# Optimization experiments

Measured on AMD Instinct MI355X. Metric: run time of the kernel, lower is better.

The kernel has to match this reference:

```python
import jax, jax.numpy as jnp
import numpy as np

B, A, T, NMODE, H = 4, 16, 32, 8, 256
NSCENE = 512
HEADS = 8
FF = 128
LN_EPS = 1e-6

def _layer_norm(x, g, b, eps=LN_EPS):
    mu = jnp.mean(x, axis=-1, keepdims=True)
    var = jnp.mean((x - mu) ** 2, axis=-1, keepdims=True)
    return (x - mu) * jax.lax.rsqrt(var + eps) * g + b


def setup_inputs() -> dict:
    key = jax.random.key(0)
    ks = jax.random.split(key, 16)
    s = 1.0 / np.sqrt(H)
    sf = 1.0 / np.sqrt(FF)
    return {
        "hidden_vecs": jax.random.normal(ks[0], (B, A, T, NMODE, H), jnp.float32),
        "scene_hidden_vec": jax.random.normal(ks[1], (B, NSCENE, H), jnp.float32),
        # nn.MultiheadAttention packed in_proj: rows [Wq; Wk; Wv]
        "in_proj_w": jax.random.normal(ks[2], (3 * H, H), jnp.float32) * s,
        "in_proj_b": jnp.zeros((3 * H,), jnp.float32),
        "out_proj_w": jax.random.normal(ks[3], (H, H), jnp.float32) * s,
        "out_proj_b": jnp.zeros((H,), jnp.float32),
        "attn_ln_g": jnp.ones((H,), jnp.float32),
        "attn_ln_b": jnp.zeros((H,), jnp.float32),
        "ff1_w": jax.random.normal(ks[4], (FF, H), jnp.float32) * s,
        "ff1_b": jnp.zeros((FF,), jnp.float32),
        "ff2_w": jax.random.normal(ks[5], (H, FF), jnp.float32) * sf,
        "ff2_b": jnp.zeros((H,), jnp.float32),
        "ff_ln_g": jnp.ones((H,), jnp.float32),
        "ff_ln_b": jnp.zeros((H,), jnp.float32),
    }


def reference(hidden_vecs, scene_hidden_vec, in_proj_w, in_proj_b, out_proj_w,
              out_proj_b, attn_ln_g, attn_ln_b, ff1_w, ff1_b, ff2_w, ff2_b,
              ff_ln_g, ff_ln_b):
    b, a, t, n, h = hidden_vecs.shape
    N = scene_hidden_vec.shape[1]
    d = h // HEADS
    m = a * t * n  # queries per batch element

    Wq, Wk, Wv = in_proj_w[:h], in_proj_w[h:2 * h], in_proj_w[2 * h:]
    bq, bk, bv = in_proj_b[:h], in_proj_b[h:2 * h], in_proj_b[2 * h:]

    # Project queries; K/V computed ONCE per batch (shared across a,t,n) --
    # avoids materializing the (b,a,t,n,N,h) expanded tensor.
    q = (hidden_vecs.reshape(b, m, h) @ Wq.T + bq).reshape(b, m, HEADS, d)
    k = (scene_hidden_vec @ Wk.T + bk).reshape(b, N, HEADS, d)
    v = (scene_hidden_vec @ Wv.T + bv).reshape(b, N, HEADS, d)

    scale = 1.0 / np.sqrt(d)
    scores = jnp.einsum('bmed,bned->bemn', q * scale, k)  # (b, heads, m, N)
    attn = jax.nn.softmax(scores, axis=-1)
    ctx = jnp.einsum('bemn,bned->bmed', attn, v).reshape(b, m, h)
    attn_out = (ctx @ out_proj_w.T + out_proj_b).reshape(b, a, t, n, h)

    # averaged attention weights over heads (average_attn_weights=True)
    attn_score = jnp.mean(attn, axis=1).reshape(b, a, t, n, 1, N)

    x = _layer_norm(attn_out + hidden_vecs, attn_ln_g, attn_ln_b)
    ff = jax.nn.relu(x @ ff1_w.T + ff1_b) @ ff2_w.T + ff2_b
    out = _layer_norm(ff + x, ff_ln_g, ff_ln_b)
    return out, attn_score
```

## Files before the change

kernel.cpp:

```cpp
#include <hip/hip_runtime.h>
#include <hip/hip_bf16.h>

#define H 256
#define NSC 512
#define MQ 4096
#define BATCH 4

typedef __attribute__((ext_vector_type(8))) short bf16x8;
typedef __attribute__((ext_vector_type(4))) float f32x4;

__device__ __forceinline__ ushort f2bf(float x) {
    union { float f; unsigned u; } c; c.f = x;
    unsigned r = c.u + 0x7FFF + ((c.u >> 16) & 1);
    return (ushort)(r >> 16);
}
__device__ __forceinline__ unsigned pk2(float hi, float lo) {
    union { float f; unsigned u; } a, b; a.f = hi; b.f = lo;
    return __builtin_amdgcn_perm(a.u, b.u, 0x07060302u);
}
__device__ __forceinline__ uint4 cvt8f(const float* p) {
    float4 a = *(const float4*)p;
    float4 b = *(const float4*)(p + 4);
    uint4 r;
    r.x = pk2(a.y, a.x); r.y = pk2(a.w, a.z);
    r.z = pk2(b.y, b.x); r.w = pk2(b.w, b.z);
    return r;
}
#define EXP2(x) __builtin_amdgcn_exp2f(x)

template<int MODE>
__device__ __forceinline__ void gemm_body(
    ushort* As, ushort* Bs, int bx, int by,
    const float* __restrict__ Ain, const float* __restrict__ W,
    const float* __restrict__ bias,
    void* __restrict__ out, ushort* __restrict__ out2,
    int K, int N, float alpha)
{
    const int t = threadIdx.x;
    const int w = t >> 6, lane = t & 63, g = lane >> 4, l15 = lane & 15;
    const int rowBase = by * 64;
    const int colBase = bx * 256;
    const int wr = (w >> 2) * 32;
    const int wc = (w & 3) * 64;
    f32x4 acc[2][4];
    #pragma unroll
    for (int mt = 0; mt < 2; mt++)
        #pragma unroll
        for (int nt = 0; nt < 4; nt++) acc[mt][nt] = (f32x4){0.f,0.f,0.f,0.f};

    const int sr = t >> 3, skc = t & 7, sp = skc ^ (sr & 7);
    const size_t arow = (size_t)(rowBase + sr) * K + skc * 8;

    uint4 av = cvt8f(Ain + arow);
    uint4 bv[4];
    #pragma unroll
    for (int i = 0; i < 4; i++) {
        const int u = t + 512*i, br = u >> 3, bkc = u & 7;
        int brow = colBase + br; if (brow > N - 1) brow = N - 1;
        bv[i] = cvt8f(W + (size_t)brow * K + bkc*8);
    }

    for (int k0 = 0; k0 < K; k0 += 64) {
        __syncthreads();
        *(uint4*)&As[sr*64 + sp*8] = av;
        #pragma unroll
        for (int i = 0; i < 4; i++) {
            const int u = t + 512*i, br = u >> 3, bkc = u & 7, bp = bkc ^ (br & 7);
            *(uint4*)&Bs[br*64 + bp*8] = bv[i];
        }
        __syncthreads();
        if (k0 + 64 < K) {
            av = cvt8f(Ain + arow + k0 + 64);
            #pragma unroll
            for (int i = 0; i < 4; i++) {
                const int u = t + 512*i, br = u >> 3, bkc = u & 7;
                int brow = colBase + br; if (brow > N - 1) brow = N - 1;
                bv[i] = cvt8f(W + (size_t)brow * K + k0 + 64 + bkc*8);
            }
        }
        #pragma unroll
        for (int kk = 0; kk < 2; kk++) {
            const int swz = ((kk*4 + g) ^ (l15 & 7)) * 8;
            bf16x8 af[2], bfr[4];
            #pragma unroll
            for (int mt = 0; mt < 2; mt++)
                af[mt] = *(const bf16x8*)&As[(wr + mt*16 + l15)*64 + swz];
            #pragma unroll
            for (int nt = 0; nt < 4; nt++)
                bfr[nt] = *(const bf16x8*)&Bs[(wc + nt*16 + l15)*64 + swz];
            #pragma unroll
            for (int mt = 0; mt < 2; mt++)
                #pragma unroll
                for (int nt = 0; nt < 4; nt++)
                    acc[mt][nt] = __builtin_amdgcn_mfma_f32_16x16x32_bf16(
                        af[mt], bfr[nt], acc[mt][nt], 0, 0, 0);
        }
    }

    if (MODE == 0) {
        #pragma unroll
        for (int nt = 0; nt < 4; nt++) {
            const int col = colBase + wc + nt*16 + l15;
            if (col < N) {
                const float bb = bias[col];
                #pragma unroll
                for (int mt = 0; mt < 2; mt++)
                    #pragma unroll
                    for (int r = 0; r < 4; r++) {
                        const int row = rowBase + wr + mt*16 + g*4 + r;
                        float o = (acc[mt][nt][r] + bb) * alpha;
                        ((ushort*)out)[(size_t)row * N + col] = f2bf(o);
                    }
            }
        }
    } else {
        #pragma unroll
        for (int nt = 0; nt < 4; nt++) {
            const int col = colBase + wc + nt*16 + l15;
            const float bb = bias[col];
            #pragma unroll
            for (int mt = 0; mt < 2; mt++) {
                const int row0 = rowBase + wr + mt*16 + g*4;
                if (col < 256) {
                    #pragma unroll
                    for (int r = 0; r < 4; r++)
                        ((ushort*)out)[(size_t)(row0 + r) * 256 + col] = f2bf(acc[mt][nt][r] + bb);
                } else {
                    ushort4 pkv = { f2bf(acc[mt][nt][0] + bb), f2bf(acc[mt][nt][1] + bb),
                                    f2bf(acc[mt][nt][2] + bb), f2bf(acc[mt][nt][3] + bb) };
                    *(ushort4*)&out2[(size_t)((row0 >> 9)*256 + col - 256) * 512 + (row0 & 511)] = pkv;
                }
            }
        }
    }
}

__global__ __launch_bounds__(512, 4) void qkv_kernel(
    const float* __restrict__ hidden, const float* __restrict__ scene,
    const float* __restrict__ in_w, const float* __restrict__ in_b,
    ushort* __restrict__ qb, ushort* __restrict__ kb, ushort* __restrict__ vtb,
    float alpha_q)
{
    __shared__ ushort As[64 * 64];
    __shared__ ushort Bs[256 * 64];
    if (blockIdx.x < 256) {
        gemm_body<0>(As, Bs, 0, blockIdx.x, hidden, in_w, in_b,
                     qb, nullptr, 256, 256, alpha_q);
    } else {
        const int bid = blockIdx.x - 256;
        gemm_body<1>(As, Bs, bid >> 5, bid & 31, scene, in_w + 65536, in_b + 256,
                     kb, vtb, 256, 512, 1.f);
    }
}

__global__ __launch_bounds__(1024, 4) void mega_kernel(
    const ushort* __restrict__ q, const ushort* __restrict__ k,
    const ushort* __restrict__ vt,
    const float* __restrict__ Wo, const float* __restrict__ bo,
    const float* __restrict__ hid,
    const float* __restrict__ ag, const float* __restrict__ ab,
    const float* __restrict__ W1, const float* __restrict__ b1,
    const float* __restrict__ W2, const float* __restrict__ b2,
    const float* __restrict__ fg, const float* __restrict__ fbv,
    float* __restrict__ out, float* __restrict__ attn_score)
{
    __shared__ uint4 SHraw[8096];
    ushort* SH = (ushort*)SHraw;
    ushort* Ks = SH;
    ushort* Vs = SH + 8448;
    ushort* Pb = SH + 18688;
    ushort* Cb = SH + 39168;
    float*  Lg = (float*)(SH + 63744);
    ushort* Bs = SH;
    ushort* Xb = SH + 18688;
    float*  Ls = (float*)(SH + 35072);
    float*  Lq = (float*)(SH + 35584);
    ushort* Fb = SH + 55552;

    const int t = threadIdx.x;
    const int w = t >> 6, lane = t & 63, g = lane >> 4, l15 = lane & 15;
    const int b = blockIdx.x >> 6;
    const int m0 = (blockIdx.x & 63) * 64;
    const size_t rowG = (size_t)b * MQ + m0;
    const size_t kg = (size_t)b * NSC * H;
    const size_t vg = (size_t)b * H * NSC;

    const int hh0 = w & 7, hf = w >> 3;
    bf16x8 qf[2];
    #pragma unroll
    for (int qt = 0; qt < 2; qt++)
        qf[qt] = *(const bf16x8*)&q[(rowG + hf*32 + qt*16 + l15) * H + hh0*32 + g*8];

    f32x4 cacc[2][2];
    float lacc[2][4];
    #pragma unroll
    for (int qt = 0; qt < 2; qt++) {
        #pragma unroll
        for (int dt = 0; dt < 2; dt++) cacc[qt][dt] = (f32x4){0.f,0.f,0.f,0.f};
        #pragma unroll
        for (int r = 0; r < 4; r++) lacc[qt][r] = 0.f;
    }

    const int skey = t >> 5, spart = t & 31;
    const int sd = t >> 2, sp2 = t & 3;
    bf16x8 kr = *(const bf16x8*)&k[kg + (size_t)skey*H + spart*8];
    bf16x8 vr = *(const bf16x8*)&vt[vg + (size_t)sd*NSC + sp2*8];

    for (int c = 0; c < 16; c++) {
        const int kbase = c * 32;
        __syncthreads();
        *(bf16x8*)&Ks[skey*264 + spart*8] = kr;
        *(bf16x8*)&Vs[sd*40 + sp2*8] = vr;
        __syncthreads();
        if (c < 15) {
            kr = *(const bf16x8*)&k[kg + (size_t)(kbase + 32 + skey)*H + spart*8];
            vr = *(const bf16x8*)&vt[vg + (size_t)sd*NSC + kbase + 32 + sp2*8];
        }
        #pragma unroll
        for (int qt = 0; qt < 2; qt++) {
            #pragma unroll
            for (int kt = 0; kt < 2; kt++) {
                bf16x8 kf = *(const bf16x8*)&Ks[(kt*16 + l15)*264 + hh0*32 + g*8];
                f32x4 s = __builtin_amdgcn_mfma_f32_16x16x32_bf16(
                    qf[qt], kf, (f32x4){0.f,0.f,0.f,0.f}, 0, 0, 0);
                #pragma unroll
                for (int r = 0; r < 4; r++) {
                    float p = EXP2(s[r]);
                    lacc[qt][r] += p;
                    Pb[(w*32 + qt*16 + g*4 + r)*40 + kt*16 + l15] = f2bf(p);
                }
            }
        }
        #pragma unroll
        for (int qt = 0; qt < 2; qt++) {
            bf16x8 pf = *(const bf16x8*)&Pb[(w*32 + qt*16 + l15)*40 + g*8];
            #pragma unroll
            for (int dt = 0; dt < 2; dt++) {
                bf16x8 vf = *(const bf16x8*)&Vs[(hh0*32 + dt*16 + l15)*40 + g*8];
                cacc[qt][dt] = __builtin_amdgcn_mfma_f32_16x16x32_bf16(
                    pf, vf, cacc[qt][dt], 0, 0, 0);
            }
        }
    }

    #pragma unroll
    for (int qt = 0; qt < 2; qt++) {
        float invl[4];
        #pragma unroll
        for (int r = 0; r < 4; r++) {
            float v = lacc[qt][r];
            v += __shfl_xor(v, 1); v += __shfl_xor(v, 2);
            v += __shfl_xor(v, 4); v += __shfl_xor(v, 8);
            invl[r] = 1.f / v;
            if (l15 == 0) Lg[hh0*64 + hf*32 + qt*16 + g*4 + r] = -__log2f(v) - 3.0f;
        }
        #pragma unroll
        for (int dt = 0; dt < 2; dt++)
            #pragma unroll
            for (int r = 0; r < 4; r++) {
                const int qr = hf*32 + qt*16 + g*4 + r;
                const int col = hh0*32 + dt*16 + l15;
                Cb[qr*256 + (((col >> 3) ^ (qr & 7)) << 3) + (col & 7)]
                    = f2bf(cacc[qt][dt][r] * invl[r]);
            }
    }

    __syncthreads();

    {
        f32x4 sacc[4][2];
        #pragma unroll
        for (int qt = 0; qt < 4; qt++)
            #pragma unroll
            for (int kt = 0; kt < 2; kt++) sacc[qt][kt] = (f32x4){0.f,0.f,0.f,0.f};

        #pragma unroll 2
        for (int h = 0; h < 8; h++) {
            float lgq[4]; bf16x8 qv[4];
            #pragma unroll
            for (int qt = 0; qt < 4; qt++) {
                lgq[qt] = Lg[h*64 + qt*16 + l15];
                qv[qt] = *(const bf16x8*)&q[(rowG + qt*16 + l15) * H + h*32 + g*8];
            }
            #pragma unroll
            for (int kt = 0; kt < 2; kt++) {
                bf16x8 kf2 = *(const bf16x8*)&k[kg + (size_t)(w*32 + kt*16 + l15)*H + h*32 + g*8];
                #pragma unroll
                for (int qt = 0; qt < 4; qt++) {
                    f32x4 s = __builtin_amdgcn_mfma_f32_16x16x32_bf16(
                        kf2, qv[qt], (f32x4){0.f,0.f,0.f,0.f}, 0, 0, 0);
                    #pragma unroll
                    for (int r = 0; r < 4; r++) sacc[qt][kt][r] += EXP2(s[r] + lgq[qt]);
                }
            }
        }
        #pragma unroll
        for (int qt = 0; qt < 4; qt++)
            #pragma unroll
            for (int kt = 0; kt < 2; kt++)
                *(f32x4*)&attn_score[(rowG + qt*16 + l15)*NSC + w*32 + kt*16 + g*4]
                    = sacc[qt][kt];
    }

    const int wr = (w >> 2) * 16;
    const int wc = (w & 3) * 64;
    float xres[4][4];
    {
        f32x4 acc[4];
        #pragma unroll
        for (int nt = 0; nt < 4; nt++) acc[nt] = (f32x4){0.f,0.f,0.f,0.f};

        uint4 bv[2];
        #pragma unroll
        for (int i = 0; i < 2; i++) {
            const int u = t + 1024*i, br = u >> 3, bkc = u & 7;
            bv[i] = cvt8f(Wo + (size_t)br * 256 + bkc*8);
        }
        for (int k0 = 0; k0 < 256; k0 += 64) {
            __syncthreads();
            #pragma unroll
            for (int i = 0; i < 2; i++) {
                const int u = t + 1024*i, br = u >> 3, bkc = u & 7, bp = bkc ^ (br & 7);
                *(uint4*)&Bs[br*64 + bp*8] = bv[i];
            }
            __syncthreads();
            if (k0 < 192) {
                #pragma unroll
                for (int i = 0; i < 2; i++) {
                    const int u = t + 1024*i, br = u >> 3, bkc = u & 7;
                    bv[i] = cvt8f(Wo + (size_t)br * 256 + k0 + 64 + bkc*8);
                }
            }
            #pragma unroll
            for (int kk = 0; kk < 2; kk++) {
                const int rowC = wr + l15;
                const int gi = (k0 >> 3) + kk*4 + g;
                bf16x8 af = *(const bf16x8*)&Cb[rowC*256 + ((gi ^ (rowC & 7)) << 3)];
                const int swz = ((kk*4 + g) ^ (l15 & 7)) * 8;
                #pragma unroll
                for (int nt = 0; nt < 4; nt++) {
                    bf16x8 bfr = *(const bf16x8*)&Bs[(wc + nt*16 + l15)*64 + swz];
                    acc[nt] = __builtin_amdgcn_mfma_f32_16x16x32_bf16(
                        af, bfr, acc[nt], 0, 0, 0);
                }
            }
        }
        float bb[4], gmv[4], btv[4];
        #pragma unroll
        for (int nt = 0; nt < 4; nt++) {
            const int col = wc + nt*16 + l15;
            bb[nt] = bo[col]; gmv[nt] = ag[col]; btv[nt] = ab[col];
        }
        #pragma unroll
        for (int r = 0; r < 4; r++) {
            const float* rp = hid + (rowG + wr + g*4 + r) * 256;
            #pragma unroll
            for (int nt = 0; nt < 4; nt++)
                acc[nt][r] += bb[nt] + rp[wc + nt*16 + l15];
        }
        float ps[4], pq[4];
        #pragma unroll
        for (int r = 0; r < 4; r++) {
            float s = (acc[0][r] + acc[1][r]) + (acc[2][r] + acc[3][r]);
            float qq = (acc[0][r]*acc[0][r] + acc[1][r]*acc[1][r])
                     + (acc[2][r]*acc[2][r] + acc[3][r]*acc[3][r]);
            #pragma unroll
            for (int m = 1; m < 16; m <<= 1) {
                s += __shfl_xor(s, m);
                qq += __shfl_xor(qq, m);
            }
            ps[r] = s; pq[r] = qq;
        }
        if (l15 == 0) {
            #pragma unroll
            for (int r = 0; r < 4; r++) {
                const int ri = wr + g*4 + r;
                Ls[ri*4 + (w & 3)] = ps[r];
                Lq[ri*4 + (w & 3)] = pq[r];
            }
        }
        __syncthreads();
        #pragma unroll
        for (int r = 0; r < 4; r++) {
            const int ri = wr + g*4 + r;
            f32x4 sv = *(const f32x4*)&Ls[ri*4];
            f32x4 qv2 = *(const f32x4*)&Lq[ri*4];
            const float mu = (sv[0]+sv[1]+sv[2]+sv[3]) * (1.f/256.f);
            const float ex2 = (qv2[0]+qv2[1]+qv2[2]+qv2[3]) * (1.f/256.f);
            const float rs = rsqrtf(ex2 - mu*mu + 1e-6f);
            #pragma unroll
            for (int nt = 0; nt < 4; nt++) {
                const int col = wc + nt*16 + l15;
                const float o = (acc[nt][r] - mu) * rs * gmv[nt] + btv[nt];
                xres[nt][r] = o;
                Xb[ri*256 + (((col >> 3) ^ (ri & 7)) << 3) + (col & 7)] = f2bf(o);
            }
        }
    }

    {
        const int wrB = (w >> 2) * 16;
        const int wcB = (w & 3) * 32;
        f32x4 facc[2];
        #pragma unroll
        for (int nt = 0; nt < 2; nt++) facc[nt] = (f32x4){0.f,0.f,0.f,0.f};

        uint4 bv2 = cvt8f(W1 + (size_t)(t >> 3) * 256 + (t & 7)*8);
        for (int k0 = 0; k0 < 256; k0 += 64) {
            __syncthreads();
            {
                const int br = t >> 3, bkc = t & 7, bp = bkc ^ (br & 7);
                *(uint4*)&Bs[br*64 + bp*8] = bv2;
            }
            __syncthreads();
            if (k0 < 192)
                bv2 = cvt8f(W1 + (size_t)(t >> 3) * 256 + k0 + 64 + (t & 7)*8);
            #pragma unroll
            for (int kk = 0; kk < 2; kk++) {
                const int rowX = wrB + l15;
                const int gi = (k0 >> 3) + kk*4 + g;
                bf16x8 af = *(const bf16x8*)&Xb[rowX*256 + ((gi ^ (rowX & 7)) << 3)];
                const int swz = ((kk*4 + g) ^ (l15 & 7)) * 8;
                #pragma unroll
                for (int nt = 0; nt < 2; nt++) {
                    bf16x8 bfr = *(const bf16x8*)&Bs[(wcB + nt*16 + l15)*64 + swz];
                    facc[nt] = __builtin_amdgcn_mfma_f32_16x16x32_bf16(
                        af, bfr, facc[nt], 0, 0, 0);
                }
            }
        }
        #pragma unroll
        for (int nt = 0; nt < 2; nt++) {
            const int colF = wcB + nt*16 + l15;
            const float fbb = b1[colF];
            #pragma unroll
            for (int r = 0; r < 4; r++) {
                const int rowF = wrB + g*4 + r;
                const float o = fmaxf(facc[nt][r] + fbb, 0.f);
                Fb[rowF*128 + (((colF >> 3) ^ (rowF & 7)) << 3) + (colF & 7)] = f2bf(o);
            }
        }
        __syncthreads();
    }

    {
        f32x4 acc2[4];
        #pragma unroll
        for (int nt = 0; nt < 4; nt++) acc2[nt] = (f32x4){0.f,0.f,0.f,0.f};

        uint4 bv3[2];
        #pragma unroll
        for (int i = 0; i < 2; i++) {
            const int u = t + 1024*i, br = u >> 3, bkc = u & 7;
            bv3[i] = cvt8f(W2 + (size_t)br * 128 + bkc*8);
        }
        for (int k0 = 0; k0 < 128; k0 += 64) {
            __syncthreads();
            #pragma unroll
            for (int i = 0; i < 2; i++) {
                const int u = t + 1024*i, br = u >> 3, bkc = u & 7, bp = bkc ^ (br & 7);
                *(uint4*)&Bs[br*64 + bp*8] = bv3[i];
            }
            __syncthreads();
            if (k0 == 0) {
                #pragma unroll
                for (int i = 0; i < 2; i++) {
                    const int u = t + 1024*i, br = u >> 3, bkc = u & 7;
                    bv3[i] = cvt8f(W2 + (size_t)br * 128 + 64 + bkc*8);
                }
            }
            #pragma unroll
            for (int kk = 0; kk < 2; kk++) {
                const int gi = (k0 >> 3) + kk*4 + g;
                const int rowF = wr + l15;
                bf16x8 af2 = *(const bf16x8*)&Fb[rowF*128 + ((gi ^ (rowF & 7)) << 3)];
                const int swz = ((kk*4 + g) ^ (l15 & 7)) * 8;
                #pragma unroll
                for (int nt = 0; nt < 4; nt++) {
                    bf16x8 bfr = *(const bf16x8*)&Bs[(wc + nt*16 + l15)*64 + swz];
                    acc2[nt] = __builtin_amdgcn_mfma_f32_16x16x32_bf16(
                        af2, bfr, acc2[nt], 0, 0, 0);
                }
            }
        }
        float bb[4], gmv[4], btv[4];
        #pragma unroll
        for (int nt = 0; nt < 4; nt++) {
            const int col = wc + nt*16 + l15;
            bb[nt] = b2[col]; gmv[nt] = fg[col]; btv[nt] = fbv[col];
        }
        #pragma unroll
        for (int r = 0; r < 4; r++)
            #pragma unroll
            for (int nt = 0; nt < 4; nt++)
                acc2[nt][r] += bb[nt] + xres[nt][r];
        float ps[4], pq[4];
        #pragma unroll
        for (int r = 0; r < 4; r++) {
            float s = (acc2[0][r] + acc2[1][r]) + (acc2[2][r] + acc2[3][r]);
            float qq = (acc2[0][r]*acc2[0][r] + acc2[1][r]*acc2[1][r])
                     + (acc2[2][r]*acc2[2][r] + acc2[3][r]*acc2[3][r]);
            #pragma unroll
            for (int m = 1; m < 16; m <<= 1) {
                s += __shfl_xor(s, m);
                qq += __shfl_xor(qq, m);
            }
            ps[r] = s; pq[r] = qq;
        }
        __syncthreads();
        if (l15 == 0) {
            #pragma unroll
            for (int r = 0; r < 4; r++) {
                const int ri = wr + g*4 + r;
                Ls[ri*4 + (w & 3)] = ps[r];
                Lq[ri*4 + (w & 3)] = pq[r];
            }
        }
        __syncthreads();
        #pragma unroll
        for (int r = 0; r < 4; r++) {
            const int ri = wr + g*4 + r;
            f32x4 sv = *(const f32x4*)&Ls[ri*4];
            f32x4 qv2 = *(const f32x4*)&Lq[ri*4];
            const float mu = (sv[0]+sv[1]+sv[2]+sv[3]) * (1.f/256.f);
            const float ex2 = (qv2[0]+qv2[1]+qv2[2]+qv2[3]) * (1.f/256.f);
            const float rs = rsqrtf(ex2 - mu*mu + 1e-6f);
            #pragma unroll
            for (int nt = 0; nt < 4; nt++) {
                const int col = wc + nt*16 + l15;
                out[(rowG + ri) * 256 + col] =
                    (acc2[nt][r] - mu) * rs * gmv[nt] + btv[nt];
            }
        }
    }
}

extern "C" void kernel_launch(void* const* d_in, const int* in_sizes, int n_in,
                              void* d_out, int out_size, void* d_ws, size_t ws_size,
                              hipStream_t stream)
{
    const float* hidden = (const float*)d_in[0];
    const float* scene  = (const float*)d_in[1];
    const float* in_w   = (const float*)d_in[2];
    const float* in_b   = (const float*)d_in[3];
    const float* out_w  = (const float*)d_in[4];
    const float* out_b  = (const float*)d_in[5];
    const float* aln_g  = (const float*)d_in[6];
    const float* aln_b  = (const float*)d_in[7];
    const float* ff1_w  = (const float*)d_in[8];
    const float* ff1_b  = (const float*)d_in[9];
    const float* ff2_w  = (const float*)d_in[10];
    const float* ff2_b  = (const float*)d_in[11];
    const float* fln_g  = (const float*)d_in[12];
    const float* fln_b  = (const float*)d_in[13];

    float* out0  = (float*)d_out;
    float* score = out0 + (size_t)BATCH * MQ * H;

    ushort* qb   = (ushort*)d_ws;
    ushort* kb   = qb   + 4194304;
    ushort* vtb  = kb   + 524288;

    const float alpha_q = 0.25507609683638066f;

    qkv_kernel<<<dim3(320), dim3(512), 0, stream>>>(
        hidden, scene, in_w, in_b, qb, kb, vtb, alpha_q);
    mega_kernel<<<dim3(256), dim3(1024), 0, stream>>>(
        qb, kb, vtb,
        out_w, out_b, hidden, aln_g, aln_b,
        ff1_w, ff1_b, ff2_w, ff2_b, fln_g, fln_b,
        out0, score);
}
```

Measured before the change: 179.4 us.

## Fuse Q projection into attention mega kernel, keep Q tile in LDS

The Q projection GEMM moves out of the separate qkv kernel and into the start of the mega kernel. Each block now projects its own 64 query rows into a swizzled bf16 tile in shared memory and reads Q from there, both for attention and for the score recompute. This removes the global write and re-read of the bf16 Q tensor and cuts the first kernel down to K/V only. In exchange, shared memory per block grows, an extra barrier is added, and Wq is loaded redundantly by every block.

```diff
diff --git a/kernel.cpp b/kernel.cpp
--- a/kernel.cpp
+++ b/kernel.cpp
@@ -97,85 +97,64 @@
         }
     }
 
-    if (MODE == 0) {
-        #pragma unroll
-        for (int nt = 0; nt < 4; nt++) {
-            const int col = colBase + wc + nt*16 + l15;
-            if (col < N) {
-                const float bb = bias[col];
-                #pragma unroll
-                for (int mt = 0; mt < 2; mt++)
-                    #pragma unroll
-                    for (int r = 0; r < 4; r++) {
-                        const int row = rowBase + wr + mt*16 + g*4 + r;
-                        float o = (acc[mt][nt][r] + bb) * alpha;
-                        ((ushort*)out)[(size_t)row * N + col] = f2bf(o);
-                    }
-            }
-        }
-    } else {
-        #pragma unroll
-        for (int nt = 0; nt < 4; nt++) {
-            const int col = colBase + wc + nt*16 + l15;
-            const float bb = bias[col];
-            #pragma unroll
-            for (int mt = 0; mt < 2; mt++) {
-                const int row0 = rowBase + wr + mt*16 + g*4;
-                if (col < 256) {
-                    #pragma unroll
-                    for (int r = 0; r < 4; r++)
-                        ((ushort*)out)[(size_t)(row0 + r) * 256 + col] = f2bf(acc[mt][nt][r] + bb);
-                } else {
-                    ushort4 pkv = { f2bf(acc[mt][nt][0] + bb), f2bf(acc[mt][nt][1] + bb),
-                                    f2bf(acc[mt][nt][2] + bb), f2bf(acc[mt][nt][3] + bb) };
-                    *(ushort4*)&out2[(size_t)((row0 >> 9)*256 + col - 256) * 512 + (row0 & 511)] = pkv;
-                }
+    #pragma unroll
+    for (int nt = 0; nt < 4; nt++) {
+        const int col = colBase + wc + nt*16 + l15;
+        const float bb = bias[col];
+        #pragma unroll
+        for (int mt = 0; mt < 2; mt++) {
+            const int row0 = rowBase + wr + mt*16 + g*4;
+            if (col < 256) {
+                #pragma unroll
+                for (int r = 0; r < 4; r++)
+                    ((ushort*)out)[(size_t)(row0 + r) * 256 + col] = f2bf(acc[mt][nt][r] + bb);
+            } else {
+                ushort4 pkv = { f2bf(acc[mt][nt][0] + bb), f2bf(acc[mt][nt][1] + bb),
+                                f2bf(acc[mt][nt][2] + bb), f2bf(acc[mt][nt][3] + bb) };
+                *(ushort4*)&out2[(size_t)((row0 >> 9)*256 + col - 256) * 512 + (row0 & 511)] = pkv;
             }
         }
     }
 }
 
-__global__ __launch_bounds__(512, 4) void qkv_kernel(
-    const float* __restrict__ hidden, const float* __restrict__ scene,
+__global__ __launch_bounds__(512, 4) void kv_kernel(
+    const float* __restrict__ scene,
     const float* __restrict__ in_w, const float* __restrict__ in_b,
-    ushort* __restrict__ qb, ushort* __restrict__ kb, ushort* __restrict__ vtb,
-    float alpha_q)
+    ushort* __restrict__ kb, ushort* __restrict__ vtb)
 {
     __shared__ ushort As[64 * 64];
     __shared__ ushort Bs[256 * 64];
-    if (blockIdx.x < 256) {
-        gemm_body<0>(As, Bs, 0, blockIdx.x, hidden, in_w, in_b,
-                     qb, nullptr, 256, 256, alpha_q);
-    } else {
-        const int bid = blockIdx.x - 256;
-        gemm_body<1>(As, Bs, bid >> 5, bid & 31, scene, in_w + 65536, in_b + 256,
-                     kb, vtb, 256, 512, 1.f);
-    }
+    gemm_body<1>(As, Bs, blockIdx.x >> 5, blockIdx.x & 31,
+                 scene, in_w + 65536, in_b + 256, kb, vtb, 256, 512, 1.f);
 }
 
 __global__ __launch_bounds__(1024, 4) void mega_kernel(
-    const ushort* __restrict__ q, const ushort* __restrict__ k,
-    const ushort* __restrict__ vt,
+    const float* __restrict__ hidden,
+    const float* __restrict__ Wq, const float* __restrict__ bq,
+    const ushort* __restrict__ k, const ushort* __restrict__ vt,
     const float* __restrict__ Wo, const float* __restrict__ bo,
-    const float* __restrict__ hid,
     const float* __restrict__ ag, const float* __restrict__ ab,
     const float* __restrict__ W1, const float* __restrict__ b1,
     const float* __restrict__ W2, const float* __restrict__ b2,
     const float* __restrict__ fg, const float* __restrict__ fbv,
-    float* __restrict__ out, float* __restrict__ attn_score)
+    float* __restrict__ out, float* __restrict__ attn_score,
+    float alpha_q)
 {
-    __shared__ uint4 SHraw[8096];
+    __shared__ uint4 SHraw[9120];
     ushort* SH = (ushort*)SHraw;
-    ushort* Ks = SH;
-    ushort* Vs = SH + 8448;
-    ushort* Pb = SH + 18688;
-    ushort* Cb = SH + 39168;
-    float*  Lg = (float*)(SH + 63744);
-    ushort* Bs = SH;
-    ushort* Xb = SH + 18688;
-    float*  Ls = (float*)(SH + 35072);
-    float*  Lq = (float*)(SH + 35584);
-    ushort* Fb = SH + 55552;
+    ushort* Ks  = SH;
+    ushort* Vs  = SH + 8448;
+    ushort* Pb  = SH + 18688;
+    ushort* As0 = SH;
+    ushort* Bs0 = SH + 4096;
+    ushort* Bs  = SH;
+    ushort* Xb  = SH + 16384;
+    float*  Ls  = (float*)(SH + 32768);
+    float*  Lq  = (float*)(SH + 33280);
+    ushort* Qb  = SH + 39168;
+    ushort* Fb  = SH + 39168;
+    ushort* Cb  = SH + 55552;
+    float*  Lg  = (float*)(SH + 71936);
 
     const int t = threadIdx.x;
     const int w = t >> 6, lane = t & 63, g = lane >> 4, l15 = lane & 15;
@@ -185,11 +164,74 @@
     const size_t kg = (size_t)b * NSC * H;
     const size_t vg = (size_t)b * H * NSC;
 
+    const int wr = (w >> 2) * 16;
+    const int wc = (w & 3) * 64;
+
+    {
+        f32x4 acc[4];
+        #pragma unroll
+        for (int nt = 0; nt < 4; nt++) acc[nt] = (f32x4){0.f,0.f,0.f,0.f};
+
+        const int sr = t >> 3, skc = t & 7, sp = skc ^ (sr & 7);
+        uint4 av;
+        if (t < 512) av = cvt8f(hidden + (rowG + sr) * 256 + skc*8);
+        uint4 bv[2];
+        #pragma unroll
+        for (int i = 0; i < 2; i++) {
+            const int u = t + 1024*i, br = u >> 3, bkc = u & 7;
+            bv[i] = cvt8f(Wq + (size_t)br * 256 + bkc*8);
+        }
+        for (int k0 = 0; k0 < 256; k0 += 64) {
+            __syncthreads();
+            if (t < 512) *(uint4*)&As0[sr*64 + sp*8] = av;
+            #pragma unroll
+            for (int i = 0; i < 2; i++) {
+                const int u = t + 1024*i, br = u >> 3, bkc = u & 7, bp = bkc ^ (br & 7);
+                *(uint4*)&Bs0[br*64 + bp*8] = bv[i];
+            }
+            __syncthreads();
+            if (k0 < 192) {
+                if (t < 512) av = cvt8f(hidden + (rowG + sr) * 256 + k0 + 64 + skc*8);
+                #pragma unroll
+                for (int i = 0; i < 2; i++) {
+                    const int u = t + 1024*i, br = u >> 3, bkc = u & 7;
+                    bv[i] = cvt8f(Wq + (size_t)br * 256 + k0 + 64 + bkc*8);
+                }
+            }
+            #pragma unroll
+            for (int kk = 0; kk < 2; kk++) {
+                const int swz = ((kk*4 + g) ^ (l15 & 7)) * 8;
+                bf16x8 af = *(const bf16x8*)&As0[(wr + l15)*64 + swz];
+                #pragma unroll
+                for (int nt = 0; nt < 4; nt++) {
+                    bf16x8 bfr = *(const bf16x8*)&Bs0[(wc + nt*16 + l15)*64 + swz];
+                    acc[nt] = __builtin_amdgcn_mfma_f32_16x16x32_bf16(
+                        af, bfr, acc[nt], 0, 0, 0);
+                }
+            }
+        }
+        #pragma unroll
+        for (int nt = 0; nt < 4; nt++) {
+            const int col = wc + nt*16 + l15;
+            const float bb = bq[col];
+            #pragma unroll
+            for (int r = 0; r < 4; r++) {
+                const int qr = wr + g*4 + r;
+                const float o = (acc[nt][r] + bb) * alpha_q;
+                Qb[qr*256 + (((col >> 3) ^ (qr & 7)) << 3) + (col & 7)] = f2bf(o);
+            }
+        }
+    }
+    __syncthreads();
+
     const int hh0 = w & 7, hf = w >> 3;
     bf16x8 qf[2];
     #pragma unroll
-    for (int qt = 0; qt < 2; qt++)
-        qf[qt] = *(const bf16x8*)&q[(rowG + hf*32 + qt*16 + l15) * H + hh0*32 + g*8];
+    for (int qt = 0; qt < 2; qt++) {
+        const int qr0 = hf*32 + qt*16 + l15;
+        const int c0 = hh0*32 + g*8;
+        qf[qt] = *(const bf16x8*)&Qb[qr0*256 + (((c0 >> 3) ^ (qr0 & 7)) << 3)];
+    }
 
     f32x4 cacc[2][2];
     float lacc[2][4];
@@ -280,7 +322,9 @@
             #pragma unroll
             for (int qt = 0; qt < 4; qt++) {
                 lgq[qt] = Lg[h*64 + qt*16 + l15];
-                qv[qt] = *(const bf16x8*)&q[(rowG + qt*16 + l15) * H + h*32 + g*8];
+                const int qr0 = qt*16 + l15;
+                const int c0 = h*32 + g*8;
+                qv[qt] = *(const bf16x8*)&Qb[qr0*256 + (((c0 >> 3) ^ (qr0 & 7)) << 3)];
             }
             #pragma unroll
             for (int kt = 0; kt < 2; kt++) {
@@ -302,8 +346,6 @@
                     = sacc[qt][kt];
     }
 
-    const int wr = (w >> 2) * 16;
-    const int wc = (w & 3) * 64;
     float xres[4][4];
     {
         f32x4 acc[4];
@@ -353,7 +395,7 @@
         }
         #pragma unroll
         for (int r = 0; r < 4; r++) {
-            const float* rp = hid + (rowG + wr + g*4 + r) * 256;
+            const float* rp = hidden + (rowG + wr + g*4 + r) * 256;
             #pragma unroll
             for (int nt = 0; nt < 4; nt++)
                 acc[nt][r] += bb[nt] + rp[wc + nt*16 + l15];
@@ -429,6 +471,7 @@
                 }
             }
         }
+        __syncthreads();
         #pragma unroll
         for (int nt = 0; nt < 2; nt++) {
             const int colF = wcB + nt*16 + l15;
@@ -557,17 +600,15 @@
     float* out0  = (float*)d_out;
     float* score = out0 + (size_t)BATCH * MQ * H;
 
-    ushort* qb   = (ushort*)d_ws;
-    ushort* kb   = qb   + 4194304;
-    ushort* vtb  = kb   + 524288;
+    ushort* kb   = (ushort*)d_ws;
+    ushort* vtb  = kb + 524288;
 
     const float alpha_q = 0.25507609683638066f;
 
-    qkv_kernel<<<dim3(320), dim3(512), 0, stream>>>(
-        hidden, scene, in_w, in_b, qb, kb, vtb, alpha_q);
+    kv_kernel<<<dim3(64), dim3(512), 0, stream>>>(scene, in_w, in_b, kb, vtb);
     mega_kernel<<<dim3(256), dim3(1024), 0, stream>>>(
-        qb, kb, vtb,
-        out_w, out_b, hidden, aln_g, aln_b,
+        hidden, in_w, in_b, kb, vtb,
+        out_w, out_b, aln_g, aln_b,
         ff1_w, ff1_b, ff2_w, ff2_b, fln_g, fln_b,
-        out0, score);
+        out0, score, alpha_q);
 }
```

Measured after the change: 167.2 us. 1.07x faster.
